# Kernel tuning notes

Measured on AMD Instinct MI355X. Metric: run time of the kernel, lower is better.

Reference implementation:

```python
import jax, jax.numpy as jnp
import numpy as np

B, T, N, F_IN, F_OUT = 8, 16, 512, 128, 64
NEG_INF = -9e15


def setup_inputs() -> dict:
    key = jax.random.key(0)
    k1, k2, k3, k4, k5 = jax.random.split(key, 5)
    x = jax.random.normal(k1, (B, T, N, F_IN), dtype=jnp.float32)
    # nn.Linear weights: FC_W [out, in], FC_a [1, 2*out], no bias
    W = jax.random.normal(k2, (F_OUT, F_IN), dtype=jnp.float32) * 0.05
    a = jax.random.normal(k3, (1, 2 * F_OUT), dtype=jnp.float32) * 0.05
    adj = jax.random.randint(k4, (N, N), 0, 2, dtype=jnp.int32)
    adj_we = jax.random.uniform(k5, (N, N), dtype=jnp.float32)
    return {"x": x, "W": W, "a": a, "adj": adj, "adj_we": adj_we}


def reference(x, W, a, adj, adj_we):
    fout = W.shape[0]
    # h = FC_W(input): [B,T,N,Fout]
    h = jnp.einsum("btnf,of->btno", x, W)
    # Additive GAT score decomposition: e[i,j] = LeakyReLU(a1.h_i + a2.h_j)
    # (equivalent to FC_a(cat([h_i, h_j])) without materializing [B,T,N,N,2F])
    a1 = a[0, :fout]
    a2 = a[0, fout:]
    src = jnp.einsum("btno,o->btn", h, a1)  # contribution of node i (repeated rows)
    dst = jnp.einsum("btno,o->btn", h, a2)  # contribution of node j (tiled rows)
    e = jax.nn.leaky_relu(src[..., :, None] + dst[..., None, :], negative_slope=0.01)
    # mask where adj <= 0, scale by edge weights, softmax over neighbors (dim=3)
    att = jnp.where(adj > 0, e, NEG_INF)
    att = att * adj_we
    att = jax.nn.softmax(att, axis=-1)
    # h_prime = attention @ h : [B,T,N,N] @ [B,T,N,Fout]
    return jnp.einsum("btij,btjo->btio", att, h)
```

## Files before the change

kernel.cpp:

```cpp
#include <hip/hip_runtime.h>
#include <hip/hip_bf16.h>

#define BTOT 128
#define NN   512
#define FIN  128
#define FOUT 64

typedef __attribute__((ext_vector_type(8))) short bf16x8;
typedef __attribute__((ext_vector_type(4))) float f32x4;

static __device__ inline ushort f2bf(float f) {
    __hip_bfloat16 h = __float2bfloat16(f);
    return *(ushort*)&h;
}
static __device__ inline float bf2f(ushort u) {
    uint v = (uint)u << 16;
    return __uint_as_float(v);
}

__global__ void k_prep(const float* __restrict__ W, const int* __restrict__ adj,
                       const float* __restrict__ we, ushort* __restrict__ Whi,
                       ushort* __restrict__ Wlo, uint* __restrict__ cd) {
    int b = blockIdx.x;
    if (b >= 256) {
        int i = (b - 256) * 256 + threadIdx.x;
        float w = W[i];
        ushort hi = f2bf(w);
        Whi[i] = hi;
        Wlo[i] = f2bf(w - bf2f(hi));
        return;
    }
    int i = (b * 256 + threadIdx.x) * 4;
    int4   a4 = *(const int4*)&adj[i];
    float4 w4 = *(const float4*)&we[i];
    uint o[4];
#pragma unroll
    for (int e = 0; e < 4; ++e) {
        bool  cn = ((const int*)&a4)[e] > 0;
        float w  = ((const float*)&w4)[e];
        ushort cb = cn ? f2bf(w * 1.44269504f) : (ushort)0;
        ushort db = (!cn && w > 0.f) ? (ushort)0xFF80 : (ushort)0;
        o[e] = ((uint)cb << 16) | db;
    }
    *(uint4*)&cd[i] = *(uint4*)&o[0];
}

__global__ void k_feat(const float* __restrict__ x, const ushort* __restrict__ Whi,
                       const ushort* __restrict__ Wlo, const float* __restrict__ a,
                       ushort* __restrict__ ht, float* __restrict__ srcv,
                       float* __restrict__ dstv) {
    const int t    = threadIdx.x;
    const int bt   = blockIdx.y;
    const int wv   = t >> 6, lane = t & 63;
    const int r    = lane & 15;
    const int kc   = lane >> 4;
    const int n0   = blockIdx.x * 64 + wv * 16;

    const float* xrow = x + ((long)bt * NN + n0 + r) * FIN;

    f32x4 acc[4] = {{0,0,0,0},{0,0,0,0},{0,0,0,0},{0,0,0,0}};

#pragma unroll
    for (int ks = 0; ks < 4; ++ks) {
        float4 xa = *(const float4*)&xrow[ks * 32 + kc * 8];
        float4 xb = *(const float4*)&xrow[ks * 32 + kc * 8 + 4];
        float xv[8] = {xa.x, xa.y, xa.z, xa.w, xb.x, xb.y, xb.z, xb.w};
        bf16x8 Ahi, Alo;
#pragma unroll
        for (int e = 0; e < 8; ++e) {
            uint b = __float_as_uint(xv[e]);
            float hf = __uint_as_float(b & 0xFFFF0000u);
            Ahi[e] = (short)(b >> 16);
            float rr = xv[e] - hf;
            Alo[e] = (short)(__float_as_uint(rr) >> 16);
        }
#pragma unroll
        for (int g = 0; g < 4; ++g) {
            const int wo = (g * 16 + r) * FIN + ks * 32 + kc * 8;
            bf16x8 Bhi = *(const bf16x8*)&Whi[wo];
            bf16x8 Blo = *(const bf16x8*)&Wlo[wo];
            acc[g] = __builtin_amdgcn_mfma_f32_16x16x32_bf16(Ahi, Bhi, acc[g], 0, 0, 0);
            acc[g] = __builtin_amdgcn_mfma_f32_16x16x32_bf16(Alo, Bhi, acc[g], 0, 0, 0);
            acc[g] = __builtin_amdgcn_mfma_f32_16x16x32_bf16(Ahi, Blo, acc[g], 0, 0, 0);
        }
    }

    float a1g[4], a2g[4];
#pragma unroll
    for (int g = 0; g < 4; ++g) {
        a1g[g] = a[g * 16 + r];
        a2g[g] = a[FOUT + g * 16 + r];
    }
    f32x4 s1v = {0,0,0,0}, s2v = {0,0,0,0};
#pragma unroll
    for (int g = 0; g < 4; ++g)
#pragma unroll
        for (int reg = 0; reg < 4; ++reg) {
            s1v[reg] += acc[g][reg] * a1g[g];
            s2v[reg] += acc[g][reg] * a2g[g];
        }
#pragma unroll
    for (int off = 8; off; off >>= 1)
#pragma unroll
        for (int reg = 0; reg < 4; ++reg) {
            s1v[reg] += __shfl_down(s1v[reg], off, 16);
            s2v[reg] += __shfl_down(s2v[reg], off, 16);
        }
    if (r == 0) {
        float4 o1 = make_float4(s1v[0], s1v[1], s1v[2], s1v[3]);
        float4 o2 = make_float4(s2v[0], s2v[1], s2v[2], s2v[3]);
        *(float4*)&srcv[bt * NN + n0 + kc * 4] = o1;
        *(float4*)&dstv[bt * NN + n0 + kc * 4] = o2;
    }

#pragma unroll
    for (int g = 0; g < 4; ++g) {
        uint2 pk;
        pk.x = (uint)f2bf(acc[g][0]) | ((uint)f2bf(acc[g][1]) << 16);
        pk.y = (uint)f2bf(acc[g][2]) | ((uint)f2bf(acc[g][3]) << 16);
        *(uint2*)&ht[(long)bt * (FOUT * NN) + (g * 16 + r) * NN + n0 + kc * 4] = pk;
    }
}

__global__ void k_attn(const ushort* __restrict__ ht, const float* __restrict__ srcv,
                       const float* __restrict__ dstv, const uint* __restrict__ cd,
                       float* __restrict__ out) {
    __shared__ ushort ps[64 * 72];
    __shared__ ushort hs[64 * 72];
    __shared__ float dst_s[NN];
    __shared__ float src_s[64];

    const int t    = threadIdx.x;
    const int bid  = blockIdx.x;
    const int bt   = bid & 127;
    const int i0   = (bid >> 7) << 6;
    const int lane = t & 63;
    const int wv   = t >> 6;

    if (t < 64) src_s[t] = srcv[bt * NN + i0 + t];
    for (int r = t; r < NN; r += 256) dst_s[r] = dstv[bt * NN + r];

    const int pi = t >> 2;
    const int pj = (t & 3) * 16;
    const uint* cdr   = cd + (i0 + pi) * NN;
    const ushort* htb = ht + (long)bt * (FOUT * NN);

    f32x4 acc0 = {0,0,0,0}, acc1 = {0,0,0,0}, acc2 = {0,0,0,0},
          acc3 = {0,0,0,0}, accd = {0,0,0,0};

    bf16x8 ones;
#pragma unroll
    for (int j = 0; j < 8; ++j) ones[j] = (short)0x3F80;

    __syncthreads();
    const float si = src_s[pi];

    const int arow = (wv * 16 + (lane & 15)) * 72;
    const int koff = (lane >> 4) * 8;

    for (int jt = 0; jt < 8; ++jt) {
        const int j0 = jt * 64;

#pragma unroll
        for (int q = 0; q < 2; ++q) {
            int idx = 2 * t + q;
            int row = idx >> 3, c8 = idx & 7;
            float4 v = *(const float4*)&htb[row * NN + j0 + c8 * 8];
            *(float4*)&hs[row * 72 + c8 * 8] = v;
        }

        ushort pu[16];
#pragma unroll
        for (int q = 0; q < 4; ++q) {
            uint4  c4  = *(const uint4*)&cdr[j0 + pj + 4 * q];
            float4 dv4 = *(const float4*)&dst_s[j0 + pj + 4 * q];
#pragma unroll
            for (int e = 0; e < 4; ++e) {
                uint  wd = ((const uint*)&c4)[e];
                float cf = __uint_as_float(wd & 0xFFFF0000u);
                float df = __uint_as_float(wd << 16);
                float s  = si + ((const float*)&dv4)[e];
                float lr = fmaxf(s, 0.01f * s);
                pu[4 * q + e] = f2bf(__builtin_amdgcn_exp2f(fmaf(cf, lr, df)));
            }
        }
        *(float4*)&ps[pi * 72 + pj]     = *(float4*)&pu[0];
        *(float4*)&ps[pi * 72 + pj + 8] = *(float4*)&pu[8];
        __syncthreads();

#pragma unroll
        for (int s2 = 0; s2 < 2; ++s2) {
            bf16x8 afr = *(bf16x8*)&ps[arow + s2 * 32 + koff];
            bf16x8 b0  = *(bf16x8*)&hs[( 0 + (lane & 15)) * 72 + s2 * 32 + koff];
            bf16x8 b1  = *(bf16x8*)&hs[(16 + (lane & 15)) * 72 + s2 * 32 + koff];
            bf16x8 b2  = *(bf16x8*)&hs[(32 + (lane & 15)) * 72 + s2 * 32 + koff];
            bf16x8 b3  = *(bf16x8*)&hs[(48 + (lane & 15)) * 72 + s2 * 32 + koff];
            acc0 = __builtin_amdgcn_mfma_f32_16x16x32_bf16(afr, b0, acc0, 0, 0, 0);
            acc1 = __builtin_amdgcn_mfma_f32_16x16x32_bf16(afr, b1, acc1, 0, 0, 0);
            acc2 = __builtin_amdgcn_mfma_f32_16x16x32_bf16(afr, b2, acc2, 0, 0, 0);
            acc3 = __builtin_amdgcn_mfma_f32_16x16x32_bf16(afr, b3, acc3, 0, 0, 0);
            accd = __builtin_amdgcn_mfma_f32_16x16x32_bf16(afr, ones, accd, 0, 0, 0);
        }
        __syncthreads();
    }

    const int orow = wv * 16 + (lane >> 4) * 4;
    const int ocol = lane & 15;
    float* ob = out + ((long)bt * NN + i0) * FOUT;
#pragma unroll
    for (int reg = 0; reg < 4; ++reg) {
        float inv = 1.0f / accd[reg];
        ob[(orow + reg) * FOUT +  0 + ocol] = acc0[reg] * inv;
        ob[(orow + reg) * FOUT + 16 + ocol] = acc1[reg] * inv;
        ob[(orow + reg) * FOUT + 32 + ocol] = acc2[reg] * inv;
        ob[(orow + reg) * FOUT + 48 + ocol] = acc3[reg] * inv;
    }
}

extern "C" void kernel_launch(void* const* d_in, const int* in_sizes, int n_in,
                              void* d_out, int out_size, void* d_ws, size_t ws_size,
                              hipStream_t stream) {
    const float* x      = (const float*)d_in[0];
    const float* W      = (const float*)d_in[1];
    const float* a      = (const float*)d_in[2];
    const int*   adj    = (const int*)d_in[3];
    const float* adj_we = (const float*)d_in[4];
    float* out = (float*)d_out;

    ushort* Whi  = (ushort*)d_ws;
    ushort* Wlo  = Whi + FOUT * FIN;
    ushort* ht   = Wlo + FOUT * FIN;
    float*  srcv = (float*)(ht + BTOT * FOUT * NN);
    float*  dstv = srcv + BTOT * NN;
    uint*   cdw  = (uint*)(dstv + BTOT * NN);

    hipLaunchKernelGGL(k_prep, dim3(288), dim3(256), 0, stream,
                       W, adj, adj_we, Whi, Wlo, cdw);
    hipLaunchKernelGGL(k_feat, dim3(8, 128), dim3(256), 0, stream,
                       x, Whi, Wlo, a, ht, srcv, dstv);
    hipLaunchKernelGGL(k_attn, dim3(1024), dim3(256), 0, stream,
                       ht, srcv, dstv, cdw, out);
}
```

Before: 51.07 us.

## Build attention MFMA A-fragments in registers and stage h in 256-column halves

Each lane now computes its own bf16 attention A-fragment directly in registers from the packed coefficient/mask data, so the P tile no longer goes through shared memory. The h tile is staged in two 256-column halves with an XOR swizzle instead of eight 64-column tiles, which cuts block-wide barriers from 16 to 4. Coefficient loads are register-prefetched one step ahead, and launch bounds are added. The trade-off is a larger shared footprint (32KB for h), which may limit occupancy, plus more register pressure from the prefetch buffers.

Measured after the change: 55.22 us. 1.08x slower.

```diff
diff --git a/kernel.cpp b/kernel.cpp
--- a/kernel.cpp
+++ b/kernel.cpp
@@ -122,13 +122,28 @@
     }
 }
 
-__global__ void k_attn(const ushort* __restrict__ ht, const float* __restrict__ srcv,
-                       const float* __restrict__ dstv, const uint* __restrict__ cd,
-                       float* __restrict__ out) {
-    __shared__ ushort ps[64 * 72];
-    __shared__ ushort hs[64 * 72];
+static __device__ inline bf16x8 make_afrag(uint4 ca, uint4 cb, float4 d0, float4 d1,
+                                           float si) {
+    float dv[8] = {d0.x, d0.y, d0.z, d0.w, d1.x, d1.y, d1.z, d1.w};
+    uint  cw[8] = {ca.x, ca.y, ca.z, ca.w, cb.x, cb.y, cb.z, cb.w};
+    bf16x8 A;
+#pragma unroll
+    for (int e = 0; e < 8; ++e) {
+        float cf = __uint_as_float(cw[e] & 0xFFFF0000u);
+        float df = __uint_as_float(cw[e] << 16);
+        float s  = si + dv[e];
+        float lr = fmaxf(s, 0.01f * s);
+        A[e] = (short)f2bf(__builtin_amdgcn_exp2f(fmaf(cf, lr, df)));
+    }
+    return A;
+}
+
+__global__ __launch_bounds__(256, 4)
+void k_attn(const ushort* __restrict__ ht, const float* __restrict__ srcv,
+            const float* __restrict__ dstv, const uint* __restrict__ cd,
+            float* __restrict__ out) {
+    __shared__ ushort hs[64 * 256];
     __shared__ float dst_s[NN];
-    __shared__ float src_s[64];
 
     const int t    = threadIdx.x;
     const int bid  = blockIdx.x;
@@ -136,72 +151,76 @@
     const int i0   = (bid >> 7) << 6;
     const int lane = t & 63;
     const int wv   = t >> 6;
-
-    if (t < 64) src_s[t] = srcv[bt * NN + i0 + t];
-    for (int r = t; r < NN; r += 256) dst_s[r] = dstv[bt * NN + r];
-
-    const int pi = t >> 2;
-    const int pj = (t & 3) * 16;
-    const uint* cdr   = cd + (i0 + pi) * NN;
+    const int r16  = lane & 15;
+    const int kq   = lane >> 4;
+    const int koff = kq * 8;
+    const int xr   = r16 & 7;
+
+    const int ri = i0 + wv * 16 + r16;
+    const float si = srcv[bt * NN + ri];
+    const uint* cdr   = cd + ri * NN;
     const ushort* htb = ht + (long)bt * (FOUT * NN);
+
+    for (int q = t; q < NN; q += 256) dst_s[q] = dstv[bt * NN + q];
 
     f32x4 acc0 = {0,0,0,0}, acc1 = {0,0,0,0}, acc2 = {0,0,0,0},
           acc3 = {0,0,0,0}, accd = {0,0,0,0};
-
     bf16x8 ones;
 #pragma unroll
     for (int j = 0; j < 8; ++j) ones[j] = (short)0x3F80;
 
-    __syncthreads();
-    const float si = src_s[pi];
-
-    const int arow = (wv * 16 + (lane & 15)) * 72;
-    const int koff = (lane >> 4) * 8;
-
-    for (int jt = 0; jt < 8; ++jt) {
-        const int j0 = jt * 64;
-
-#pragma unroll
-        for (int q = 0; q < 2; ++q) {
-            int idx = 2 * t + q;
-            int row = idx >> 3, c8 = idx & 7;
-            float4 v = *(const float4*)&htb[row * NN + j0 + c8 * 8];
-            *(float4*)&hs[row * 72 + c8 * 8] = v;
-        }
-
-        ushort pu[16];
-#pragma unroll
-        for (int q = 0; q < 4; ++q) {
-            uint4  c4  = *(const uint4*)&cdr[j0 + pj + 4 * q];
-            float4 dv4 = *(const float4*)&dst_s[j0 + pj + 4 * q];
-#pragma unroll
-            for (int e = 0; e < 4; ++e) {
-                uint  wd = ((const uint*)&c4)[e];
-                float cf = __uint_as_float(wd & 0xFFFF0000u);
-                float df = __uint_as_float(wd << 16);
-                float s  = si + ((const float*)&dv4)[e];
-                float lr = fmaxf(s, 0.01f * s);
-                pu[4 * q + e] = f2bf(__builtin_amdgcn_exp2f(fmaf(cf, lr, df)));
+    for (int half = 0; half < 2; ++half) {
+        __syncthreads();
+#pragma unroll
+        for (int q = 0; q < 8; ++q) {
+            int idx = q * 256 + t;
+            int o = idx >> 5, c8 = idx & 31;
+            float4 v = *(const float4*)&htb[(o << 9) + (half << 8) + (c8 << 3)];
+            *(float4*)&hs[(o << 8) + ((c8 ^ (o & 7)) << 3)] = v;
+        }
+        __syncthreads();
+
+        const int jg = half * 256;
+        uint4 cA0 = *(const uint4*)&cdr[jg + koff];
+        uint4 cA1 = *(const uint4*)&cdr[jg + koff + 4];
+        uint4 cB0 = *(const uint4*)&cdr[jg + 32 + koff];
+        uint4 cB1 = *(const uint4*)&cdr[jg + 32 + koff + 4];
+
+#pragma unroll
+        for (int jtl = 0; jtl < 4; ++jtl) {
+            const int jgc = jg + jtl * 64;
+            uint4 nA0 = {0,0,0,0}, nA1 = {0,0,0,0}, nB0 = {0,0,0,0}, nB1 = {0,0,0,0};
+            if (jtl < 3) {
+                nA0 = *(const uint4*)&cdr[jgc + 64 + koff];
+                nA1 = *(const uint4*)&cdr[jgc + 64 + koff + 4];
+                nB0 = *(const uint4*)&cdr[jgc + 96 + koff];
+                nB1 = *(const uint4*)&cdr[jgc + 96 + koff + 4];
             }
-        }
-        *(float4*)&ps[pi * 72 + pj]     = *(float4*)&pu[0];
-        *(float4*)&ps[pi * 72 + pj + 8] = *(float4*)&pu[8];
-        __syncthreads();
-
-#pragma unroll
-        for (int s2 = 0; s2 < 2; ++s2) {
-            bf16x8 afr = *(bf16x8*)&ps[arow + s2 * 32 + koff];
-            bf16x8 b0  = *(bf16x8*)&hs[( 0 + (lane & 15)) * 72 + s2 * 32 + koff];
-            bf16x8 b1  = *(bf16x8*)&hs[(16 + (lane & 15)) * 72 + s2 * 32 + koff];
-            bf16x8 b2  = *(bf16x8*)&hs[(32 + (lane & 15)) * 72 + s2 * 32 + koff];
-            bf16x8 b3  = *(bf16x8*)&hs[(48 + (lane & 15)) * 72 + s2 * 32 + koff];
-            acc0 = __builtin_amdgcn_mfma_f32_16x16x32_bf16(afr, b0, acc0, 0, 0, 0);
-            acc1 = __builtin_amdgcn_mfma_f32_16x16x32_bf16(afr, b1, acc1, 0, 0, 0);
-            acc2 = __builtin_amdgcn_mfma_f32_16x16x32_bf16(afr, b2, acc2, 0, 0, 0);
-            acc3 = __builtin_amdgcn_mfma_f32_16x16x32_bf16(afr, b3, acc3, 0, 0, 0);
-            accd = __builtin_amdgcn_mfma_f32_16x16x32_bf16(afr, ones, accd, 0, 0, 0);
-        }
-        __syncthreads();
+            float4 d00 = *(float4*)&dst_s[jgc + koff];
+            float4 d01 = *(float4*)&dst_s[jgc + koff + 4];
+            float4 d10 = *(float4*)&dst_s[jgc + 32 + koff];
+            float4 d11 = *(float4*)&dst_s[jgc + 32 + koff + 4];
+
+            bf16x8 A0 = make_afrag(cA0, cA1, d00, d01, si);
+            bf16x8 A1 = make_afrag(cB0, cB1, d10, d11, si);
+
+#pragma unroll
+            for (int s2 = 0; s2 < 2; ++s2) {
+                bf16x8 A = s2 ? A1 : A0;
+                const int c8v = jtl * 8 + s2 * 4 + kq;
+                const int cs  = (c8v ^ xr) << 3;
+                bf16x8 b0 = *(bf16x8*)&hs[(( 0 + r16) << 8) + cs];
+                bf16x8 b1 = *(bf16x8*)&hs[((16 + r16) << 8) + cs];
+                bf16x8 b2 = *(bf16x8*)&hs[((32 + r16) << 8) + cs];
+                bf16x8 b3 = *(bf16x8*)&hs[((48 + r16) << 8) + cs];
+                acc0 = __builtin_amdgcn_mfma_f32_16x16x32_bf16(A, b0, acc0, 0, 0, 0);
+                acc1 = __builtin_amdgcn_mfma_f32_16x16x32_bf16(A, b1, acc1, 0, 0, 0);
+                acc2 = __builtin_amdgcn_mfma_f32_16x16x32_bf16(A, b2, acc2, 0, 0, 0);
+                acc3 = __builtin_amdgcn_mfma_f32_16x16x32_bf16(A, b3, acc3, 0, 0, 0);
+                accd = __builtin_amdgcn_mfma_f32_16x16x32_bf16(A, ones, accd, 0, 0, 0);
+            }
+            cA0 = nA0; cA1 = nA1; cB0 = nB0; cB1 = nB1;
+        }
     }
 
     const int orow = wv * 16 + (lane >> 4) * 4;
```
